# Kernel optimization log

Measured on AMD Instinct MI355X. Metric: run time of the kernel, lower is better.

The kernel has to match this reference:

```python
import jax, jax.numpy as jnp
import numpy as np

H = 2048  # hid_dim
D = 2048  # input_dim (gru input size)
L = 256   # input_len


def setup_inputs() -> dict:
    key = jax.random.key(0)
    ks = jax.random.split(key, 16)
    s_pre = 1.0 / np.sqrt(7)
    s_gru = 1.0 / np.sqrt(H)
    s_out = 1.0 / np.sqrt(H)
    return {
        "timepoints": jax.random.uniform(ks[0], (L, 1), jnp.float32),
        "pk_data": jax.random.normal(ks[1], (L, 1), jnp.float32),
        "input_len": L,
        "emb_patient": 5,
        "drug_route": jax.random.uniform(ks[2], (1,), jnp.float32),
        "dose": jax.random.uniform(ks[3], (1,), jnp.float32),
        "smiles": jax.random.normal(ks[4], (1, H), jnp.float32),
        "tf_mask": jax.random.randint(ks[5], (L,), 0, 2, jnp.int32),
        "emb_table": jax.random.normal(ks[6], (8, 3), jnp.float32),
        "W_pre": jax.random.uniform(ks[7], (D, 7), jnp.float32, -s_pre, s_pre),
        "b_pre": jax.random.uniform(ks[8], (D,), jnp.float32, -s_pre, s_pre),
        "W_ih": jax.random.uniform(ks[9], (3 * H, D), jnp.float32, -s_gru, s_gru),
        "W_hh": jax.random.uniform(ks[10], (3 * H, H), jnp.float32, -s_gru, s_gru),
        "b_ih": jax.random.uniform(ks[11], (3 * H,), jnp.float32, -s_gru, s_gru),
        "b_hh": jax.random.uniform(ks[12], (3 * H,), jnp.float32, -s_gru, s_gru),
        "W_out": jax.random.uniform(ks[13], (1, H), jnp.float32, -s_out, s_out),
        "b_out": jax.random.uniform(ks[14], (1,), jnp.float32, -s_out, s_out),
    }


def _gru_cell(x, h, W_ih, W_hh, b_ih, b_hh):
    # PyTorch GRUCell math. x: [D], h: [H]
    gi = W_ih @ x + b_ih            # [3H]
    gh = W_hh @ h + b_hh            # [3H]
    i_r, i_z, i_n = jnp.split(gi, 3)
    h_r, h_z, h_n = jnp.split(gh, 3)
    r = jax.nn.sigmoid(i_r + h_r)
    z = jax.nn.sigmoid(i_z + h_z)
    n = jnp.tanh(i_n + r * h_n)
    return (1.0 - z) * n + z * h


def reference(timepoints, pk_data, input_len, emb_patient, drug_route, dose,
              smiles, tf_mask, emb_table, W_pre, b_pre, W_ih, W_hh, b_ih,
              b_hh, W_out, b_out):
    add_info = jnp.concatenate([emb_table[emb_patient], drug_route])  # [4]
    h0 = smiles[0]          # [H]
    pk0 = pk_data[0]        # [1]

    def step(carry, xs):
        pk, h = carry
        tp_prev, pk_teach, tf = xs
        x7 = jnp.concatenate([pk, tp_prev, dose, add_info])  # [7]
        x = W_pre @ x7 + b_pre                               # [D]
        h = _gru_cell(x, h, W_ih, W_hh, b_ih, b_hh)          # [H]
        pred = W_out @ h + b_out                             # [1]
        pk_next = jnp.where(tf == 1, pred, pk_teach)
        return (pk_next, h), pred

    xs = (timepoints[:-1], pk_data[1:], tf_mask[1:])
    _, preds = jax.lax.scan(step, (pk0, h0), xs)             # [L-1, 1]
    outputs = jnp.concatenate([pk0[None, :], preds], axis=0)  # [L, 1]
    return outputs
```

## Files before the change

kernel.cpp:

```cpp
#include <hip/hip_runtime.h>
#include <math.h>

#define Hdim 2048
#define Ldim 256
#define NBLK 256
#define TPB  1024
#define JPB  8
#define NREP 8

typedef unsigned long long u64;

#define WS_HP 0

__device__ __forceinline__ float fast_sigmoid(float x) {
    return __builtin_amdgcn_rcpf(1.0f + __expf(-x));
}
__device__ __forceinline__ float fast_tanh(float x) {
    return 1.0f - 2.0f * __builtin_amdgcn_rcpf(1.0f + __expf(2.0f * x));
}

__global__ __launch_bounds__(TPB, 4) void gru_all(
    const float* __restrict__ Whh,  const float* __restrict__ bhh,
    const float* __restrict__ Wout, const float* __restrict__ bout,
    const float* __restrict__ tps,  const float* __restrict__ pkdata,
    const int*   __restrict__ tf,   const float* __restrict__ smiles,
    const float* __restrict__ Wp,   const float* __restrict__ bpre,
    const float* __restrict__ Wih,  const float* __restrict__ bih,
    const float* __restrict__ dose, const float* __restrict__ route,
    const float* __restrict__ emb,  const int* __restrict__ pat,
    float* __restrict__ ws, float* __restrict__ out)
{
    const int b    = blockIdx.x;
    const int tid  = threadIdx.x;
    const int k    = tid & 127;
    const int g    = tid >> 7;
    const int wv   = tid >> 6;
    const int lane = tid & 63;
    const int j    = b*JPB + g;
    const int rep  = b & 7;

    __shared__ float su[Hdim];
    __shared__ float sh_h[Hdim];
    __shared__ float sred[16][4];
    __shared__ float sfin[16];
    __shared__ float sA[24], sT[24], sC[24];
    __shared__ float s_tp[Ldim];
    __shared__ float s_pkd[Ldim];
    __shared__ int   s_tf[Ldim];

    unsigned* hq = (unsigned*)(ws + WS_HP);

    for (int i = tid; i < Ldim; i += TPB) {
        s_tp[i]  = tps[i];
        s_pkd[i] = pkdata[i];
        s_tf[i]  = tf[i];
    }

    {
        float d = dose[0], rt = route[0];
        int p = pat[0];
        float e0 = emb[p*3+0], e1 = emb[p*3+1], e2 = emb[p*3+2];
        for (int i = tid; i < Hdim; i += TPB) {
            const float* wr = Wp + i*7;
            su[i] = d*wr[2] + e0*wr[3] + e1*wr[4] + e2*wr[5] + rt*wr[6] + bpre[i];
        }
    }

    float4 w[3][4];
    #pragma unroll
    for (int r = 0; r < 3; ++r) {
        const float* base = Whh + (size_t)(j + r*Hdim) * Hdim;
        #pragma unroll
        for (int c = 0; c < 4; ++c)
            w[r][c] = *(const float4*)(base + c*512 + k*4);
    }

    float4 wout[4];
    #pragma unroll
    for (int c = 0; c < 4; ++c)
        wout[c] = *(const float4*)(Wout + c*512 + k*4);

    const int i0 = tid * 2;
    const float wo0 = Wout[i0], wo1 = Wout[i0 + 1];
    const float bo = bout[0];

    __syncthreads();

    #pragma unroll
    for (int pass = 0; pass < 2; ++pass) {
        int ri = wv + pass*16;
        if (ri < 24) {
            int grow = (ri >> 3)*Hdim + b*JPB + (ri & 7);
            const float* wr = Wih + (size_t)grow * Hdim;
            float s0 = 0.f, s1 = 0.f, s2 = 0.f;
            #pragma unroll
            for (int c = 0; c < 8; ++c) {
                int col = c*256 + lane*4;
                float4 wv4 = *(const float4*)(wr + col);
                float4 uv4 = *(const float4*)(su + col);
                s0 += wv4.x*Wp[(col+0)*7+0] + wv4.y*Wp[(col+1)*7+0]
                    + wv4.z*Wp[(col+2)*7+0] + wv4.w*Wp[(col+3)*7+0];
                s1 += wv4.x*Wp[(col+0)*7+1] + wv4.y*Wp[(col+1)*7+1]
                    + wv4.z*Wp[(col+2)*7+1] + wv4.w*Wp[(col+3)*7+1];
                s2 += wv4.x*uv4.x + wv4.y*uv4.y + wv4.z*uv4.z + wv4.w*uv4.w;
            }
            #pragma unroll
            for (int off = 32; off >= 1; off >>= 1) {
                s0 += __shfl_down(s0, off, 64);
                s1 += __shfl_down(s1, off, 64);
                s2 += __shfl_down(s2, off, 64);
            }
            if (lane == 0) {
                sA[ri] = s0;
                sT[ri] = s1;
                sC[ri] = s2 + bih[grow];
            }
        }
    }
    __syncthreads();

    float apk_r=0, apk_z=0, apk_n=0, atp_r=0, atp_z=0, atp_n=0,
          cvt_r=0, cvt_z=0, cvt_n=0, br=0, bz=0, bn=0, hprev=0;
    if (wv == 0) {
        float hinit = 0.f;
        if (lane < JPB) {
            int jj = b*JPB + lane;
            apk_r = sA[lane]; apk_z = sA[8+lane]; apk_n = sA[16+lane];
            atp_r = sT[lane]; atp_z = sT[8+lane]; atp_n = sT[16+lane];
            cvt_r = sC[lane]; cvt_z = sC[8+lane]; cvt_n = sC[16+lane];
            br = bhh[jj]; bz = bhh[jj + Hdim]; bn = bhh[jj + 2*Hdim];
            hprev = smiles[jj];
            hinit = hprev;
        }
        float hv = __shfl(hinit, lane & 7);
        unsigned w0 = (__float_as_uint(hv) & 0xFFFFFF00u);
        __hip_atomic_store(hq + (size_t)(lane >> 3)*Hdim + b*JPB + (lane & 7), w0,
                           __ATOMIC_RELAXED, __HIP_MEMORY_SCOPE_AGENT);
        if (b == 0 && lane == 0) out[0] = pkdata[0];
    }

    for (int t = 0; t < Ldim - 1; ++t) {
        const int pr_ = t & 1;
        const unsigned* hin = hq + (size_t)(pr_*NREP + rep)*Hdim;
        const unsigned tt = (unsigned)t & 0xFFu;

        u64 q;
        for (;;) {
            q = __hip_atomic_load((const u64*)(hin + i0),
                                  __ATOMIC_RELAXED, __HIP_MEMORY_SCOPE_AGENT);
            if (((unsigned)q & 0xFFu) == tt &&
                ((unsigned)(q >> 32) & 0xFFu) == tt) break;
        }
        float h0 = __uint_as_float((unsigned)q         & 0xFFFFFF00u);
        float h1 = __uint_as_float((unsigned)(q >> 32) & 0xFFFFFF00u);
        sh_h[i0]     = h0;
        sh_h[i0 + 1] = h1;
        __syncthreads();

        float prd = 0.f, pzd = 0.f, pnd = 0.f, pwd = 0.f;
        #pragma unroll
        for (int c = 0; c < 4; ++c) {
            float4 hv4 = *(const float4*)(sh_h + c*512 + k*4);
            prd += w[0][c].x*hv4.x + w[0][c].y*hv4.y + w[0][c].z*hv4.z + w[0][c].w*hv4.w;
            pzd += w[1][c].x*hv4.x + w[1][c].y*hv4.y + w[1][c].z*hv4.z + w[1][c].w*hv4.w;
            pnd += w[2][c].x*hv4.x + w[2][c].y*hv4.y + w[2][c].z*hv4.z + w[2][c].w*hv4.w;
            pwd += wout[c].x*hv4.x + wout[c].y*hv4.y + wout[c].z*hv4.z + wout[c].w*hv4.w;
        }
        #pragma unroll
        for (int off = 32; off >= 1; off >>= 1) {
            prd += __shfl_down(prd, off, 64);
            pzd += __shfl_down(pzd, off, 64);
            pnd += __shfl_down(pnd, off, 64);
            pwd += __shfl_down(pwd, off, 64);
        }
        if (lane == 0) {
            sred[wv][0] = prd; sred[wv][1] = pzd;
            sred[wv][2] = pnd; sred[wv][3] = pwd;
        }
        __syncthreads();

        if (wv == 0) {
            __builtin_amdgcn_s_setprio(1);
            float pred = sred[0][3] + sred[1][3] + bo;
            float pk = (t == 0) ? s_pkd[0] : ((s_tf[t] == 1) ? pred : s_pkd[t]);
            float hvnew = 0.f;
            if (lane < JPB) {
                float dotr = sred[2*lane][0] + sred[2*lane+1][0];
                float dotz = sred[2*lane][1] + sred[2*lane+1][1];
                float dotn = sred[2*lane][2] + sred[2*lane+1][2];
                float tp  = s_tp[t];
                float gr  = apk_r*pk + atp_r*tp + cvt_r + dotr + br;
                float gz  = apk_z*pk + atp_z*tp + cvt_z + dotz + bz;
                float gin = apk_n*pk + atp_n*tp + cvt_n;
                float r = fast_sigmoid(gr);
                float z = fast_sigmoid(gz);
                float n = fast_tanh(gin + r*(dotn + bn));
                hvnew = (1.0f - z)*n + z*hprev;
                hprev = hvnew;
            }
            float hv = __shfl(hvnew, lane & 7);
            unsigned wpk = (__float_as_uint(hv) & 0xFFFFFF00u)
                         | ((unsigned)(t + 1) & 0xFFu);
            __hip_atomic_store(hq + (size_t)(((pr_^1)*NREP) + (lane >> 3))*Hdim
                                   + b*JPB + (lane & 7), wpk,
                               __ATOMIC_RELAXED, __HIP_MEMORY_SCOPE_AGENT);
            __builtin_amdgcn_s_setprio(0);
            if (b == 0 && lane == 0 && t > 0) out[t] = pred;
        }
    }

    if (b == 0) {
        const unsigned* hin = hq + (size_t)((((Ldim - 1) & 1))*NREP + 0)*Hdim;
        const unsigned tt = (unsigned)(Ldim - 1) & 0xFFu;
        u64 q;
        for (;;) {
            q = __hip_atomic_load((const u64*)(hin + i0),
                                  __ATOMIC_RELAXED, __HIP_MEMORY_SCOPE_AGENT);
            if (((unsigned)q & 0xFFu) == tt &&
                ((unsigned)(q >> 32) & 0xFFu) == tt) break;
        }
        float h0 = __uint_as_float((unsigned)q         & 0xFFFFFF00u);
        float h1 = __uint_as_float((unsigned)(q >> 32) & 0xFFFFFF00u);
        float wpart = wo0*h0 + wo1*h1;
        #pragma unroll
        for (int off = 32; off >= 1; off >>= 1) wpart += __shfl_down(wpart, off, 64);
        if (lane == 0) sfin[wv] = wpart;
        __syncthreads();
        if (wv == 0) {
            float s = (lane < 16) ? sfin[lane] : 0.f;
            s += __shfl_down(s, 8, 64);
            s += __shfl_down(s, 4, 64);
            s += __shfl_down(s, 2, 64);
            s += __shfl_down(s, 1, 64);
            if (lane == 0) out[Ldim - 1] = s + bo;
        }
    }
}

extern "C" void kernel_launch(void* const* d_in, const int* in_sizes, int n_in,
                              void* d_out, int out_size, void* d_ws, size_t ws_size,
                              hipStream_t stream)
{
    const float* tps    = (const float*)d_in[0];
    const float* pkdata = (const float*)d_in[1];
    const int*   pat    = (const int*)  d_in[3];
    const float* route  = (const float*)d_in[4];
    const float* dose   = (const float*)d_in[5];
    const float* smiles = (const float*)d_in[6];
    const int*   tfm    = (const int*)  d_in[7];
    const float* emb    = (const float*)d_in[8];
    const float* Wp     = (const float*)d_in[9];
    const float* bpre   = (const float*)d_in[10];
    const float* Wih    = (const float*)d_in[11];
    const float* Whh    = (const float*)d_in[12];
    const float* bih    = (const float*)d_in[13];
    const float* bhh    = (const float*)d_in[14];
    const float* Wout   = (const float*)d_in[15];
    const float* bout   = (const float*)d_in[16];
    float* out = (float*)d_out;
    float* ws  = (float*)d_ws;

    hipLaunchKernelGGL(gru_all, dim3(NBLK), dim3(TPB), 0, stream,
                       Whh, bhh, Wout, bout, tps, pkdata, tfm, smiles,
                       Wp, bpre, Wih, bih, dose, route, emb, pat, ws, out);
}
```

Before: 958.9 us.

## Replace second block barrier with LDS flags and double-buffer shared h

The second __syncthreads after the per-wave partial reductions is replaced by per-wave LDS flags that only wave 0 spins on. Other waves can then proceed straight to polling the next step's hidden state. The shared h buffer is double-buffered by step parity so early waves do not overwrite data still being read. The global poll also issues two loads in flight, which may cut spin latency but adds memory traffic and makes the ordering logic more fragile.

```diff
diff --git a/kernel.cpp b/kernel.cpp
--- a/kernel.cpp
+++ b/kernel.cpp
@@ -17,6 +17,10 @@
 }
 __device__ __forceinline__ float fast_tanh(float x) {
     return 1.0f - 2.0f * __builtin_amdgcn_rcpf(1.0f + __expf(2.0f * x));
+}
+
+__device__ __forceinline__ bool tag_ok(u64 q, unsigned tt) {
+    return ((unsigned)q & 0xFFu) == tt && ((unsigned)(q >> 32) & 0xFFu) == tt;
 }
 
 __global__ __launch_bounds__(TPB, 4) void gru_all(
@@ -40,8 +44,9 @@
     const int rep  = b & 7;
 
     __shared__ float su[Hdim];
-    __shared__ float sh_h[Hdim];
+    __shared__ float sh_h[2][Hdim];
     __shared__ float sred[16][4];
+    __shared__ unsigned sflag[16];
     __shared__ float sfin[16];
     __shared__ float sA[24], sT[24], sC[24];
     __shared__ float s_tp[Ldim];
@@ -55,6 +60,7 @@
         s_pkd[i] = pkdata[i];
         s_tf[i]  = tf[i];
     }
+    if (tid < 16) sflag[tid] = 0xFFFFFFFFu;
 
     {
         float d = dose[0], rt = route[0];
@@ -141,26 +147,25 @@
 
     for (int t = 0; t < Ldim - 1; ++t) {
         const int pr_ = t & 1;
-        const unsigned* hin = hq + (size_t)(pr_*NREP + rep)*Hdim;
+        const u64* hin64 = (const u64*)(hq + (size_t)(pr_*NREP + rep)*Hdim + i0);
         const unsigned tt = (unsigned)t & 0xFFu;
 
-        u64 q;
-        for (;;) {
-            q = __hip_atomic_load((const u64*)(hin + i0),
-                                  __ATOMIC_RELAXED, __HIP_MEMORY_SCOPE_AGENT);
-            if (((unsigned)q & 0xFFu) == tt &&
-                ((unsigned)(q >> 32) & 0xFFu) == tt) break;
-        }
-        float h0 = __uint_as_float((unsigned)q         & 0xFFFFFF00u);
-        float h1 = __uint_as_float((unsigned)(q >> 32) & 0xFFFFFF00u);
-        sh_h[i0]     = h0;
-        sh_h[i0 + 1] = h1;
+        u64 q0 = __hip_atomic_load(hin64, __ATOMIC_RELAXED, __HIP_MEMORY_SCOPE_AGENT);
+        u64 q1 = __hip_atomic_load(hin64, __ATOMIC_RELAXED, __HIP_MEMORY_SCOPE_AGENT);
+        while (!tag_ok(q0, tt)) {
+            q0 = q1;
+            q1 = __hip_atomic_load(hin64, __ATOMIC_RELAXED, __HIP_MEMORY_SCOPE_AGENT);
+        }
+        float h0 = __uint_as_float((unsigned)q0         & 0xFFFFFF00u);
+        float h1 = __uint_as_float((unsigned)(q0 >> 32) & 0xFFFFFF00u);
+        sh_h[pr_][i0]     = h0;
+        sh_h[pr_][i0 + 1] = h1;
         __syncthreads();
 
         float prd = 0.f, pzd = 0.f, pnd = 0.f, pwd = 0.f;
         #pragma unroll
         for (int c = 0; c < 4; ++c) {
-            float4 hv4 = *(const float4*)(sh_h + c*512 + k*4);
+            float4 hv4 = *(const float4*)(&sh_h[pr_][c*512 + k*4]);
             prd += w[0][c].x*hv4.x + w[0][c].y*hv4.y + w[0][c].z*hv4.z + w[0][c].w*hv4.w;
             pzd += w[1][c].x*hv4.x + w[1][c].y*hv4.y + w[1][c].z*hv4.z + w[1][c].w*hv4.w;
             pnd += w[2][c].x*hv4.x + w[2][c].y*hv4.y + w[2][c].z*hv4.z + w[2][c].w*hv4.w;
@@ -176,10 +181,18 @@
         if (lane == 0) {
             sred[wv][0] = prd; sred[wv][1] = pzd;
             sred[wv][2] = pnd; sred[wv][3] = pwd;
-        }
-        __syncthreads();
+            __hip_atomic_store(&sflag[wv], (unsigned)t,
+                               __ATOMIC_RELEASE, __HIP_MEMORY_SCOPE_WORKGROUP);
+        }
 
         if (wv == 0) {
+            for (;;) {
+                unsigned f = (lane < 16)
+                    ? __hip_atomic_load(&sflag[lane], __ATOMIC_ACQUIRE,
+                                        __HIP_MEMORY_SCOPE_WORKGROUP)
+                    : (unsigned)t;
+                if (__all(f == (unsigned)t)) break;
+            }
             __builtin_amdgcn_s_setprio(1);
             float pred = sred[0][3] + sred[1][3] + bo;
             float pk = (t == 0) ? s_pkd[0] : ((s_tf[t] == 1) ? pred : s_pkd[t]);
@@ -210,14 +223,11 @@
     }
 
     if (b == 0) {
-        const unsigned* hin = hq + (size_t)((((Ldim - 1) & 1))*NREP + 0)*Hdim;
+        const u64* hin64 = (const u64*)(hq + (size_t)(1*NREP + 0)*Hdim + i0);
         const unsigned tt = (unsigned)(Ldim - 1) & 0xFFu;
-        u64 q;
-        for (;;) {
-            q = __hip_atomic_load((const u64*)(hin + i0),
-                                  __ATOMIC_RELAXED, __HIP_MEMORY_SCOPE_AGENT);
-            if (((unsigned)q & 0xFFu) == tt &&
-                ((unsigned)(q >> 32) & 0xFFu) == tt) break;
+        u64 q = __hip_atomic_load(hin64, __ATOMIC_RELAXED, __HIP_MEMORY_SCOPE_AGENT);
+        while (!tag_ok(q, tt)) {
+            q = __hip_atomic_load(hin64, __ATOMIC_RELAXED, __HIP_MEMORY_SCOPE_AGENT);
         }
         float h0 = __uint_as_float((unsigned)q         & 0xFFFFFF00u);
         float h1 = __uint_as_float((unsigned)(q >> 32) & 0xFFFFFF00u);
```

Result: slower. 1.018 ms (+6.2%).
